# Performance work log

Measured on AMD Instinct MI355X. Metric: run time of the kernel, lower is better.

Reference implementation:

```python
import jax, jax.numpy as jnp
import numpy as np

N, DIM, HEADS, DHEAD = 4096, 1024, 16, 64
INNER = HEADS * DHEAD


def setup_inputs() -> dict:
    key = jax.random.key(0)
    ks = jax.random.split(key, 6)
    s_in = 1.0 / np.sqrt(DIM)
    s_inner = 1.0 / np.sqrt(INNER)
    return {
        "x": jax.random.normal(ks[0], (N, DIM), dtype=jnp.float32),
        # weights stored as (in, out) so y = x @ W
        "Wq": jax.random.uniform(ks[1], (DIM, INNER), jnp.float32, -s_in, s_in),
        "Wk": jax.random.uniform(ks[2], (DIM, INNER), jnp.float32, -s_in, s_in),
        "Wv": jax.random.uniform(ks[3], (DIM, INNER), jnp.float32, -s_in, s_in),
        "Wo": jax.random.uniform(ks[4], (INNER, DIM), jnp.float32, -s_inner, s_inner),
        "bo": jax.random.uniform(ks[5], (DIM,), jnp.float32, -s_inner, s_inner),
    }


def reference(x, Wq, Wk, Wv, Wo, bo):
    scale = DHEAD ** -0.5
    # [n, h, d] -> [h, n, d]
    q = (x @ Wq).reshape(N, HEADS, DHEAD).transpose(1, 0, 2)
    k = (x @ Wk).reshape(N, HEADS, DHEAD).transpose(1, 0, 2)
    v = (x @ Wv).reshape(N, HEADS, DHEAD).transpose(1, 0, 2)
    dots = jnp.einsum("hnd,hmd->hnm", q, k) * scale  # [h, n, n]
    attn = jax.nn.softmax(dots, axis=-1)
    out = jnp.einsum("hnm,hmd->hnd", attn, v)  # [h, n, d]
    out = out.transpose(1, 0, 2).reshape(N, INNER)
    return out @ Wo + bo
```

## Files before the change

### kernel.cpp

```cpp
#include <hip/hip_runtime.h>
#include <cstdint>
#include <cstddef>

typedef _Float16 f16;
typedef _Float16 f16x8 __attribute__((ext_vector_type(8)));
typedef _Float16 f16x4 __attribute__((ext_vector_type(4)));
typedef __fp16 fp16x2 __attribute__((ext_vector_type(2)));
typedef float floatx4 __attribute__((ext_vector_type(4)));
typedef float floatx16 __attribute__((ext_vector_type(16)));

constexpr int SEQ = 4096;
constexpr int DIM = 1024;
constexpr int NHEAD = 16;
constexpr int DH = 64;

#define QSCALE 0.18033688011112042f

__device__ __forceinline__ void async16(void* lds, const void* g) {
  __builtin_amdgcn_global_load_lds(
      (__attribute__((address_space(1))) void*)g,
      (__attribute__((address_space(3))) void*)lds, 16, 0, 0);
}

__device__ __forceinline__ uint32_t pk2(float a, float b) {
  union { fp16x2 h; uint32_t u; } c;
  c.h = __builtin_amdgcn_cvt_pkrtz(a, b);
  return c.u;
}

__device__ __forceinline__ float dot2acc(uint32_t packed, float acc) {
#if __has_builtin(__builtin_amdgcn_fdot2)
  union { uint32_t u; fp16x2 h; } c; c.u = packed;
  fp16x2 one2; one2.x = (__fp16)1.0f; one2.y = (__fp16)1.0f;
  return __builtin_amdgcn_fdot2(c.h, one2, acc, false);
#else
  union { uint32_t u; fp16x2 h; } c; c.u = packed;
  return acc + (float)c.h.x + (float)c.h.y;
#endif
}


__global__ void cvt_x(const float* __restrict__ x, f16* __restrict__ xh) {
  int i = (blockIdx.x * 256 + threadIdx.x) * 4;
  float4 v = *(const float4*)(x + i);
  f16x4 o;
  o.x = (f16)v.x; o.y = (f16)v.y; o.z = (f16)v.z; o.w = (f16)v.w;
  *(f16x4*)(xh + i) = o;
}

__global__ void transpose_cvt(const float* __restrict__ w0, const float* __restrict__ w1,
                              const float* __restrict__ w2, const float* __restrict__ w3,
                              f16* __restrict__ o0, f16* __restrict__ o1,
                              f16* __restrict__ o2, f16* __restrict__ o3) {
  __shared__ float tile[32][33];
  int z = blockIdx.z;
  const float* W = (z == 0) ? w0 : (z == 1) ? w1 : (z == 2) ? w2 : w3;
  f16* O = (z == 0) ? o0 : (z == 1) ? o1 : (z == 2) ? o2 : o3;
  int tx = threadIdx.x, ty = threadIdx.y;
  int xc = blockIdx.x * 32 + tx;
  for (int i = ty; i < 32; i += 8)
    tile[i][tx] = W[(size_t)(blockIdx.y * 32 + i) * DIM + xc];
  __syncthreads();
  int xo = blockIdx.y * 32 + tx;
  for (int i = ty; i < 32; i += 8)
    O[(size_t)(blockIdx.x * 32 + i) * DIM + xo] = (f16)tile[tx][i];
}

__global__ __launch_bounds__(256, 3) void gemm_qkv(
    const f16* __restrict__ xh, const f16* __restrict__ wqt,
    const f16* __restrict__ wkt, const f16* __restrict__ wvt,
    f16* __restrict__ q_ws, f16* __restrict__ k_ws, f16* __restrict__ vt_ws) {
  __shared__ f16 smem[16896];
  f16* a_lds = smem;
  f16* b_lds = smem + 4096;
  const int tid = threadIdx.x;
  const int lane = tid & 63, l16 = lane & 15, quad = lane >> 4;
  const int w = tid >> 6, wr = w >> 1, wc = w & 1;
  const int m0 = blockIdx.x * 128, n0 = blockIdx.y * 128;
  const int z = blockIdx.z;
  const f16* Bt = (z == 0) ? wqt : (z == 1) ? wkt : wvt;

  floatx4 acc[4][4];
#pragma unroll
  for (int mt = 0; mt < 4; ++mt)
#pragma unroll
    for (int nt = 0; nt < 4; ++nt) acc[mt][nt] = (floatx4){0.f, 0.f, 0.f, 0.f};

  for (int k0 = 0; k0 < DIM; k0 += 32) {
#pragma unroll
    for (int rnd = 0; rnd < 2; ++rnd) {
      int e = (rnd * 256 + tid) * 8;
      int cb = e >> 10, r = (e >> 3) & 127;
      async16(a_lds + e, xh + (size_t)(m0 + r) * DIM + k0 + cb * 8);
      async16(b_lds + e, Bt + (size_t)(n0 + r) * DIM + k0 + cb * 8);
    }
    __syncthreads();
    f16x8 af[4], bq[4];
#pragma unroll
    for (int mt = 0; mt < 4; ++mt)
      af[mt] = *(const f16x8*)(a_lds + quad * 1024 + (wr * 64 + mt * 16 + l16) * 8);
#pragma unroll
    for (int nt = 0; nt < 4; ++nt)
      bq[nt] = *(const f16x8*)(b_lds + quad * 1024 + (wc * 64 + nt * 16 + l16) * 8);
#pragma unroll
    for (int mt = 0; mt < 4; ++mt)
#pragma unroll
      for (int nt = 0; nt < 4; ++nt)
        acc[mt][nt] = __builtin_amdgcn_mfma_f32_16x16x32_f16(af[mt], bq[nt], acc[mt][nt], 0, 0, 0);
    __syncthreads();
  }

  if (z < 2) {
#pragma unroll
    for (int mt = 0; mt < 4; ++mt)
#pragma unroll
      for (int nt = 0; nt < 4; ++nt)
#pragma unroll
        for (int r = 0; r < 4; ++r) {
          int m = m0 + wr * 64 + mt * 16 + quad * 4 + r;
          int c = n0 + wc * 64 + nt * 16 + l16;
          float v = acc[mt][nt][r];
          if (z == 0)
            q_ws[(size_t)((c >> 6) * SEQ + m) * DH + (c & 63)] = (f16)(v * QSCALE);
          else
            k_ws[(size_t)((c >> 6) * SEQ + m) * DH + (c & 63)] = (f16)v;
        }
  } else {
#pragma unroll
    for (int mt = 0; mt < 4; ++mt)
#pragma unroll
      for (int nt = 0; nt < 4; ++nt)
#pragma unroll
        for (int r = 0; r < 4; ++r) {
          int cl = wc * 64 + nt * 16 + l16;
          int ml = wr * 64 + mt * 16 + quad * 4 + r;
          smem[cl * 132 + ml] = (f16)acc[mt][nt][r];
        }
    __syncthreads();
#pragma unroll
    for (int it = 0; it < 8; ++it) {
      int idx = it * 256 + tid;
      int cl = idx >> 4, mp = (idx & 15) * 8;
      f16x4 lo = *(const f16x4*)(smem + cl * 132 + mp);
      f16x4 hi4 = *(const f16x4*)(smem + cl * 132 + mp + 4);
      f16x8 v8;
#pragma unroll
      for (int j = 0; j < 4; ++j) { v8[j] = lo[j]; v8[4 + j] = hi4[j]; }
      *(f16x8*)(vt_ws + (size_t)(n0 + cl) * SEQ + m0 + mp) = v8;
    }
  }
}

__global__ __launch_bounds__(256, 4) void attn_kernel(
    const f16* __restrict__ qg, const f16* __restrict__ kg,
    const f16* __restrict__ vtg, f16* __restrict__ po, float* __restrict__ ps) {
  __shared__ f16 smem[16384];
  f16* k_lds = smem;
  f16* v_lds = smem + 8192;

  const int tid = threadIdx.x;
  const int w = tid >> 6, lane = tid & 63, l32 = lane & 31;
  const int hi = lane >> 5;
  const int h = blockIdx.y, qt = blockIdx.x, half = blockIdx.z;
  const int q0 = qt * 128 + w * 32;

  f16x8 qf[4];
#pragma unroll
  for (int kf = 0; kf < 4; ++kf)
    qf[kf] = *(const f16x8*)(qg + (size_t)(h * SEQ + q0 + l32) * DH + kf * 16 + hi * 8);

  floatx16 oacc[2];
  oacc[0] = (floatx16)0.f; oacc[1] = (floatx16)0.f;
  float ssum = 0.f;

  const int kt0 = half * (SEQ / 256), kt1 = kt0 + (SEQ / 256);
  for (int kt = kt0; kt < kt1; ++kt) {
#pragma unroll
    for (int rnd = 0; rnd < 4; ++rnd) {
      int e = (rnd * 256 + tid) * 8;
      {
        int cb = e >> 10, r = (e >> 3) & 127;
        async16(k_lds + e, kg + (size_t)(h * SEQ + kt * 128 + r) * DH + cb * 8);
      }
      {
        int cb = e >> 9, r = (e >> 3) & 63;
        async16(v_lds + e, vtg + (size_t)(h * DH + r) * SEQ + kt * 128 + cb * 8);
      }
    }
    __syncthreads();

#pragma unroll
    for (int kb = 0; kb < 4; ++kb) {
      floatx16 sacc = (floatx16)0.f;
#pragma unroll
      for (int kf = 0; kf < 4; ++kf) {
        f16x8 kfrag = *(const f16x8*)(k_lds + (kf * 2 + hi) * 1024 + (kb * 32 + l32) * 8);
        sacc = __builtin_amdgcn_mfma_f32_32x32x16_f16(kfrag, qf[kf], sacc, 0, 0, 0);
      }
      float p[16];
#pragma unroll
      for (int r = 0; r < 16; ++r) p[r] = exp2f(sacc[r]);
#pragma unroll
      for (int kh = 0; kh < 2; ++kh) {
        uint32_t d0a = pk2(p[8 * kh + 0], p[8 * kh + 1]);
        uint32_t d0b = pk2(p[8 * kh + 2], p[8 * kh + 3]);
        uint32_t d1a = pk2(p[8 * kh + 4], p[8 * kh + 5]);
        uint32_t d1b = pk2(p[8 * kh + 6], p[8 * kh + 7]);
        ssum = dot2acc(d0a, ssum);
        ssum = dot2acc(d0b, ssum);
        ssum = dot2acc(d1a, ssum);
        ssum = dot2acc(d1b, ssum);
        uint32_t ra = (uint32_t)__shfl_xor((int)(hi ? d0a : d1a), 32);
        uint32_t rb = (uint32_t)__shfl_xor((int)(hi ? d0b : d1b), 32);
        union { uint32_t u[4]; f16x8 v; } bu;
        bu.u[0] = hi ? ra : d0a;
        bu.u[1] = hi ? rb : d0b;
        bu.u[2] = hi ? d1a : ra;
        bu.u[3] = hi ? d1b : rb;
        f16x8 bfrag = bu.v;
        int cb = kb * 4 + kh * 2 + hi;
#pragma unroll
        for (int dt = 0; dt < 2; ++dt) {
          f16x8 vfrag = *(const f16x8*)(v_lds + cb * 512 + (dt * 32 + l32) * 8);
          oacc[dt] = __builtin_amdgcn_mfma_f32_32x32x16_f16(vfrag, bfrag, oacc[dt], 0, 0, 0);
        }
      }
    }
    __syncthreads();
  }

  ssum += __shfl_xor(ssum, 32);
  const int tileid = (half * NHEAD + h) * 32 + qt;
  if (hi == 0) ps[(size_t)tileid * 128 + w * 32 + l32] = ssum;

  f16* pob = po + (size_t)tileid * 8192;
#pragma unroll
  for (int dt = 0; dt < 2; ++dt)
#pragma unroll
    for (int r = 0; r < 16; ++r) {
      int d = dt * 32 + (r & 3) + 8 * (r >> 2) + 4 * hi;
      pob[d * 128 + w * 32 + l32] = (f16)oacc[dt][r];
    }
}

__global__ __launch_bounds__(256, 4) void combine(
    const f16* __restrict__ po, const float* __restrict__ ps, f16* __restrict__ og) {
  __shared__ float inv_s[128];
  __shared__ f16 t[128 * 68];
  const int tid = threadIdx.x;
  const int h = blockIdx.y, qt = blockIdx.x;
  const int t0 = h * 32 + qt, t1 = (NHEAD + h) * 32 + qt;
  if (tid < 128) inv_s[tid] = 1.f / (ps[(size_t)t0 * 128 + tid] + ps[(size_t)t1 * 128 + tid]);
  __syncthreads();
  const f16* b0 = po + (size_t)t0 * 8192;
  const f16* b1 = po + (size_t)t1 * 8192;
#pragma unroll
  for (int it = 0; it < 4; ++it) {
    int e = (it * 256 + tid) * 8;
    int d = e >> 7, q = e & 127;
    f16x8 a = *(const f16x8*)(b0 + e);
    f16x8 b = *(const f16x8*)(b1 + e);
#pragma unroll
    for (int j = 0; j < 8; ++j)
      t[(q + j) * 68 + d] = (f16)(((float)a[j] + (float)b[j]) * inv_s[q + j]);
  }
  __syncthreads();
#pragma unroll
  for (int it = 0; it < 4; ++it) {
    int idx = it * 256 + tid;
    int q = idx >> 3, dcol = (idx & 7) * 8;
    f16x4 lo = *(const f16x4*)(t + q * 68 + dcol);
    f16x4 hi4 = *(const f16x4*)(t + q * 68 + dcol + 4);
    f16x8 v8;
#pragma unroll
    for (int j = 0; j < 4; ++j) { v8[j] = lo[j]; v8[4 + j] = hi4[j]; }
    *(f16x8*)(og + (size_t)(qt * 128 + q) * DIM + h * DH + dcol) = v8;
  }
}

__global__ __launch_bounds__(256, 2) void gemm_o(
    const f16* __restrict__ ab, const f16* __restrict__ wot,
    const float* __restrict__ bo, float* __restrict__ out) {
  __shared__ f16 a_lds[4096];
  __shared__ f16 b_lds[2048];
  const int tid = threadIdx.x;
  const int lane = tid & 63, l16 = lane & 15, quad = lane >> 4;
  const int w = tid >> 6, wr = w >> 1, wc = w & 1;
  const int m0 = blockIdx.x * 128, n0 = blockIdx.y * 64;

  floatx4 acc[4][2];
#pragma unroll
  for (int mt = 0; mt < 4; ++mt)
#pragma unroll
    for (int nt = 0; nt < 2; ++nt) acc[mt][nt] = (floatx4){0.f, 0.f, 0.f, 0.f};

  for (int k0 = 0; k0 < DIM; k0 += 32) {
#pragma unroll
    for (int rnd = 0; rnd < 2; ++rnd) {
      int e = (rnd * 256 + tid) * 8;
      int cb = e >> 10, r = (e >> 3) & 127;
      async16(a_lds + e, ab + (size_t)(m0 + r) * DIM + k0 + cb * 8);
    }
    {
      int e = tid * 8;
      int cb = e >> 9, r = (e >> 3) & 63;
      async16(b_lds + e, wot + (size_t)(n0 + r) * DIM + k0 + cb * 8);
    }
    __syncthreads();
    f16x8 af[4], bq[2];
#pragma unroll
    for (int mt = 0; mt < 4; ++mt)
      af[mt] = *(const f16x8*)(a_lds + quad * 1024 + (wr * 64 + mt * 16 + l16) * 8);
#pragma unroll
    for (int nt = 0; nt < 2; ++nt)
      bq[nt] = *(const f16x8*)(b_lds + quad * 512 + (wc * 32 + nt * 16 + l16) * 8);
#pragma unroll
    for (int mt = 0; mt < 4; ++mt)
#pragma unroll
      for (int nt = 0; nt < 2; ++nt)
        acc[mt][nt] = __builtin_amdgcn_mfma_f32_16x16x32_f16(af[mt], bq[nt], acc[mt][nt], 0, 0, 0);
    __syncthreads();
  }

#pragma unroll
  for (int mt = 0; mt < 4; ++mt)
#pragma unroll
    for (int nt = 0; nt < 2; ++nt)
#pragma unroll
      for (int r = 0; r < 4; ++r) {
        int m = m0 + wr * 64 + mt * 16 + quad * 4 + r;
        int c = n0 + wc * 32 + nt * 16 + l16;
        out[(size_t)m * DIM + c] = acc[mt][nt][r] + bo[c];
      }
}


extern "C" void kernel_launch(void* const* d_in, const int* in_sizes, int n_in,
                              void* d_out, int out_size, void* d_ws, size_t ws_size,
                              hipStream_t stream) {
  (void)in_sizes; (void)n_in; (void)out_size; (void)ws_size;
  const float* x  = (const float*)d_in[0];
  const float* Wq = (const float*)d_in[1];
  const float* Wk = (const float*)d_in[2];
  const float* Wv = (const float*)d_in[3];
  const float* Wo = (const float*)d_in[4];
  const float* bo = (const float*)d_in[5];
  float* out = (float*)d_out;
  char* ws = (char*)d_ws;

  f16* xh    = (f16*)(ws);
  f16* wqt   = (f16*)(ws + (8u  << 20));
  f16* wkt   = (f16*)(ws + (10u << 20));
  f16* wvt   = (f16*)(ws + (12u << 20));
  f16* wot   = (f16*)(ws + (14u << 20));
  f16* q_ws  = (f16*)(ws + (16u << 20));
  f16* k_ws  = (f16*)(ws + (24u << 20));
  f16* vt_ws = (f16*)(ws + (32u << 20));
  f16* po    = (f16*)(ws + (40u << 20));
  float* ps  = (float*)(ws + (57u << 20));
  f16* aout  = xh;

  cvt_x<<<dim3(SEQ * DIM / 1024), dim3(256), 0, stream>>>(x, xh);
  transpose_cvt<<<dim3(32, 32, 4), dim3(32, 8), 0, stream>>>(Wq, Wk, Wv, Wo, wqt, wkt, wvt, wot);
  gemm_qkv<<<dim3(32, 8, 3), dim3(256), 0, stream>>>(xh, wqt, wkt, wvt, q_ws, k_ws, vt_ws);
  attn_kernel<<<dim3(SEQ / 128, NHEAD, 2), dim3(256), 0, stream>>>(q_ws, k_ws, vt_ws, po, ps);
  combine<<<dim3(SEQ / 128, NHEAD), dim3(256), 0, stream>>>(po, ps, aout);
  gemm_o<<<dim3(32, 16), dim3(256), 0, stream>>>(aout, wot, bo, out);
}
```

Baseline: 288.7 us.

## Shrink attention query tile to 64 and split key blocks across warps

The attention kernel now processes 64 queries per block instead of 128. Its four warps form a 2x2 grid over queries and keys, and each iteration streams a 64-key chunk. Partial outputs and softmax sums from the two key-split warps are reduced through shared memory before writing. The combine kernel is resized to match. This doubles the grid, halves LDS per block and raises occupancy. The cost is more K/V reloads per query, since each K/V tile is now shared by only 64 queries, plus an extra LDS reduction and sync at the end.

New measurement: 532.3 us. 1.84x slower.

```diff
diff --git a/kernel.cpp b/kernel.cpp
--- a/kernel.cpp
+++ b/kernel.cpp
@@ -151,113 +151,123 @@
   }
 }
 
-__global__ __launch_bounds__(256, 4) void attn_kernel(
+__global__ __launch_bounds__(256, 8) void attn_kernel(
     const f16* __restrict__ qg, const f16* __restrict__ kg,
     const f16* __restrict__ vtg, f16* __restrict__ po, float* __restrict__ ps) {
-  __shared__ f16 smem[16384];
+  __shared__ f16 smem[8448];
   f16* k_lds = smem;
-  f16* v_lds = smem + 8192;
+  f16* v_lds = smem + 4096;
 
   const int tid = threadIdx.x;
   const int w = tid >> 6, lane = tid & 63, l32 = lane & 31;
   const int hi = lane >> 5;
+  const int wq = w & 1, wk = w >> 1;
   const int h = blockIdx.y, qt = blockIdx.x, half = blockIdx.z;
-  const int q0 = qt * 128 + w * 32;
 
   f16x8 qf[4];
 #pragma unroll
   for (int kf = 0; kf < 4; ++kf)
-    qf[kf] = *(const f16x8*)(qg + (size_t)(h * SEQ + q0 + l32) * DH + kf * 16 + hi * 8);
+    qf[kf] = *(const f16x8*)(qg + (size_t)(h * SEQ + qt * 64 + wq * 32 + l32) * DH +
+                             kf * 16 + hi * 8);
 
   floatx16 oacc[2];
   oacc[0] = (floatx16)0.f; oacc[1] = (floatx16)0.f;
   float ssum = 0.f;
 
-  const int kt0 = half * (SEQ / 256), kt1 = kt0 + (SEQ / 256);
-  for (int kt = kt0; kt < kt1; ++kt) {
-#pragma unroll
-    for (int rnd = 0; rnd < 4; ++rnd) {
+  const int kk0 = half * (SEQ / 2);
+  for (int kt = 0; kt < 32; ++kt) {
+    const int kk = kk0 + kt * 64;
+#pragma unroll
+    for (int rnd = 0; rnd < 2; ++rnd) {
       int e = (rnd * 256 + tid) * 8;
-      {
-        int cb = e >> 10, r = (e >> 3) & 127;
-        async16(k_lds + e, kg + (size_t)(h * SEQ + kt * 128 + r) * DH + cb * 8);
+      int cb = e >> 9, r = (e >> 3) & 63;
+      async16(k_lds + e, kg + (size_t)(h * SEQ + kk + r) * DH + cb * 8);
+      async16(v_lds + e, vtg + (size_t)(h * DH + r) * SEQ + kk + cb * 8);
+    }
+    __syncthreads();
+
+    floatx16 sacc = (floatx16)0.f;
+#pragma unroll
+    for (int kf = 0; kf < 4; ++kf) {
+      f16x8 kfrag = *(const f16x8*)(k_lds + (kf * 2 + hi) * 512 + (wk * 32 + l32) * 8);
+      sacc = __builtin_amdgcn_mfma_f32_32x32x16_f16(kfrag, qf[kf], sacc, 0, 0, 0);
+    }
+    float p[16];
+#pragma unroll
+    for (int r = 0; r < 16; ++r) p[r] = exp2f(sacc[r]);
+#pragma unroll
+    for (int kh = 0; kh < 2; ++kh) {
+      uint32_t d0a = pk2(p[8 * kh + 0], p[8 * kh + 1]);
+      uint32_t d0b = pk2(p[8 * kh + 2], p[8 * kh + 3]);
+      uint32_t d1a = pk2(p[8 * kh + 4], p[8 * kh + 5]);
+      uint32_t d1b = pk2(p[8 * kh + 6], p[8 * kh + 7]);
+      ssum = dot2acc(d0a, ssum);
+      ssum = dot2acc(d0b, ssum);
+      ssum = dot2acc(d1a, ssum);
+      ssum = dot2acc(d1b, ssum);
+      uint32_t ra = (uint32_t)__shfl_xor((int)(hi ? d0a : d1a), 32);
+      uint32_t rb = (uint32_t)__shfl_xor((int)(hi ? d0b : d1b), 32);
+      union { uint32_t u[4]; f16x8 v; } bu;
+      bu.u[0] = hi ? ra : d0a;
+      bu.u[1] = hi ? rb : d0b;
+      bu.u[2] = hi ? d1a : ra;
+      bu.u[3] = hi ? d1b : rb;
+      f16x8 bfrag = bu.v;
+      int cb = wk * 4 + kh * 2 + hi;
+#pragma unroll
+      for (int dt = 0; dt < 2; ++dt) {
+        f16x8 vfrag = *(const f16x8*)(v_lds + cb * 512 + (dt * 32 + l32) * 8);
+        oacc[dt] = __builtin_amdgcn_mfma_f32_32x32x16_f16(vfrag, bfrag, oacc[dt], 0, 0, 0);
       }
-      {
-        int cb = e >> 9, r = (e >> 3) & 63;
-        async16(v_lds + e, vtg + (size_t)(h * DH + r) * SEQ + kt * 128 + cb * 8);
+    }
+    __syncthreads();
+  }
+
+  ssum += __shfl_xor(ssum, 32);
+
+  float* oF = (float*)smem;
+  float* ssums = oF + 4160;
+  if (wk == 1) {
+#pragma unroll
+    for (int dt = 0; dt < 2; ++dt)
+#pragma unroll
+      for (int r = 0; r < 16; ++r) {
+        int d = dt * 32 + (r & 3) + 8 * (r >> 2) + 4 * hi;
+        oF[(wq * 32 + l32) * 65 + d] = oacc[dt][r];
       }
-    }
-    __syncthreads();
-
-#pragma unroll
-    for (int kb = 0; kb < 4; ++kb) {
-      floatx16 sacc = (floatx16)0.f;
-#pragma unroll
-      for (int kf = 0; kf < 4; ++kf) {
-        f16x8 kfrag = *(const f16x8*)(k_lds + (kf * 2 + hi) * 1024 + (kb * 32 + l32) * 8);
-        sacc = __builtin_amdgcn_mfma_f32_32x32x16_f16(kfrag, qf[kf], sacc, 0, 0, 0);
+    if (hi == 0) ssums[wq * 32 + l32] = ssum;
+  }
+  __syncthreads();
+  if (wk == 0) {
+    const int tileid = (half * NHEAD + h) * 64 + qt;
+    f16* pob = po + (size_t)tileid * 4096;
+    int q = wq * 32 + l32;
+#pragma unroll
+    for (int dt = 0; dt < 2; ++dt)
+#pragma unroll
+      for (int r = 0; r < 16; ++r) {
+        int d = dt * 32 + (r & 3) + 8 * (r >> 2) + 4 * hi;
+        pob[d * 64 + q] = (f16)(oacc[dt][r] + oF[q * 65 + d]);
       }
-      float p[16];
-#pragma unroll
-      for (int r = 0; r < 16; ++r) p[r] = exp2f(sacc[r]);
-#pragma unroll
-      for (int kh = 0; kh < 2; ++kh) {
-        uint32_t d0a = pk2(p[8 * kh + 0], p[8 * kh + 1]);
-        uint32_t d0b = pk2(p[8 * kh + 2], p[8 * kh + 3]);
-        uint32_t d1a = pk2(p[8 * kh + 4], p[8 * kh + 5]);
-        uint32_t d1b = pk2(p[8 * kh + 6], p[8 * kh + 7]);
-        ssum = dot2acc(d0a, ssum);
-        ssum = dot2acc(d0b, ssum);
-        ssum = dot2acc(d1a, ssum);
-        ssum = dot2acc(d1b, ssum);
-        uint32_t ra = (uint32_t)__shfl_xor((int)(hi ? d0a : d1a), 32);
-        uint32_t rb = (uint32_t)__shfl_xor((int)(hi ? d0b : d1b), 32);
-        union { uint32_t u[4]; f16x8 v; } bu;
-        bu.u[0] = hi ? ra : d0a;
-        bu.u[1] = hi ? rb : d0b;
-        bu.u[2] = hi ? d1a : ra;
-        bu.u[3] = hi ? d1b : rb;
-        f16x8 bfrag = bu.v;
-        int cb = kb * 4 + kh * 2 + hi;
-#pragma unroll
-        for (int dt = 0; dt < 2; ++dt) {
-          f16x8 vfrag = *(const f16x8*)(v_lds + cb * 512 + (dt * 32 + l32) * 8);
-          oacc[dt] = __builtin_amdgcn_mfma_f32_32x32x16_f16(vfrag, bfrag, oacc[dt], 0, 0, 0);
-        }
-      }
-    }
-    __syncthreads();
-  }
-
-  ssum += __shfl_xor(ssum, 32);
-  const int tileid = (half * NHEAD + h) * 32 + qt;
-  if (hi == 0) ps[(size_t)tileid * 128 + w * 32 + l32] = ssum;
-
-  f16* pob = po + (size_t)tileid * 8192;
-#pragma unroll
-  for (int dt = 0; dt < 2; ++dt)
-#pragma unroll
-    for (int r = 0; r < 16; ++r) {
-      int d = dt * 32 + (r & 3) + 8 * (r >> 2) + 4 * hi;
-      pob[d * 128 + w * 32 + l32] = (f16)oacc[dt][r];
-    }
-}
-
-__global__ __launch_bounds__(256, 4) void combine(
+    if (hi == 0) ps[(size_t)tileid * 64 + q] = ssum + ssums[q];
+  }
+}
+
+__global__ __launch_bounds__(256, 8) void combine(
     const f16* __restrict__ po, const float* __restrict__ ps, f16* __restrict__ og) {
-  __shared__ float inv_s[128];
-  __shared__ f16 t[128 * 68];
+  __shared__ float inv_s[64];
+  __shared__ f16 t[64 * 68];
   const int tid = threadIdx.x;
   const int h = blockIdx.y, qt = blockIdx.x;
-  const int t0 = h * 32 + qt, t1 = (NHEAD + h) * 32 + qt;
-  if (tid < 128) inv_s[tid] = 1.f / (ps[(size_t)t0 * 128 + tid] + ps[(size_t)t1 * 128 + tid]);
+  const int t0 = h * 64 + qt, t1 = (NHEAD + h) * 64 + qt;
+  if (tid < 64) inv_s[tid] = 1.f / (ps[(size_t)t0 * 64 + tid] + ps[(size_t)t1 * 64 + tid]);
   __syncthreads();
-  const f16* b0 = po + (size_t)t0 * 8192;
-  const f16* b1 = po + (size_t)t1 * 8192;
-#pragma unroll
-  for (int it = 0; it < 4; ++it) {
+  const f16* b0 = po + (size_t)t0 * 4096;
+  const f16* b1 = po + (size_t)t1 * 4096;
+#pragma unroll
+  for (int it = 0; it < 2; ++it) {
     int e = (it * 256 + tid) * 8;
-    int d = e >> 7, q = e & 127;
+    int d = e >> 6, q = e & 63;
     f16x8 a = *(const f16x8*)(b0 + e);
     f16x8 b = *(const f16x8*)(b1 + e);
 #pragma unroll
@@ -266,7 +276,7 @@
   }
   __syncthreads();
 #pragma unroll
-  for (int it = 0; it < 4; ++it) {
+  for (int it = 0; it < 2; ++it) {
     int idx = it * 256 + tid;
     int q = idx >> 3, dcol = (idx & 7) * 8;
     f16x4 lo = *(const f16x4*)(t + q * 68 + dcol);
@@ -274,7 +284,7 @@
     f16x8 v8;
 #pragma unroll
     for (int j = 0; j < 4; ++j) { v8[j] = lo[j]; v8[4 + j] = hi4[j]; }
-    *(f16x8*)(og + (size_t)(qt * 128 + q) * DIM + h * DH + dcol) = v8;
+    *(f16x8*)(og + (size_t)(qt * 64 + q) * DIM + h * DH + dcol) = v8;
   }
 }
 
@@ -363,7 +373,7 @@
   cvt_x<<<dim3(SEQ * DIM / 1024), dim3(256), 0, stream>>>(x, xh);
   transpose_cvt<<<dim3(32, 32, 4), dim3(32, 8), 0, stream>>>(Wq, Wk, Wv, Wo, wqt, wkt, wvt, wot);
   gemm_qkv<<<dim3(32, 8, 3), dim3(256), 0, stream>>>(xh, wqt, wkt, wvt, q_ws, k_ws, vt_ws);
-  attn_kernel<<<dim3(SEQ / 128, NHEAD, 2), dim3(256), 0, stream>>>(q_ws, k_ws, vt_ws, po, ps);
-  combine<<<dim3(SEQ / 128, NHEAD), dim3(256), 0, stream>>>(po, ps, aout);
+  attn_kernel<<<dim3(SEQ / 64, NHEAD, 2), dim3(256), 0, stream>>>(q_ws, k_ws, vt_ws, po, ps);
+  combine<<<dim3(SEQ / 64, NHEAD), dim3(256), 0, stream>>>(po, ps, aout);
   gemm_o<<<dim3(32, 16), dim3(256), 0, stream>>>(aout, wot, bo, out);
 }
```

## Split attention key tile across two wave groups with 512-thread blocks

Applied to the files above, without the earlier changes.

The attention kernel now runs 512 threads per block. Two groups of four waves each take half of every 128-key tile, which halves the serial per-wave work along the key dimension and raises waves per CU. The partial outputs and row sums of the two groups are reduced through LDS before the single global write. In exchange, each block now does an extra LDS reduction and barrier at the end, and the launch bounds change, which tightens the register budget per thread.

Result: slower. 549.2 us (+90.3%).

```diff
diff --git a/kernel.cpp b/kernel.cpp
--- a/kernel.cpp
+++ b/kernel.cpp
@@ -151,7 +151,7 @@
   }
 }
 
-__global__ __launch_bounds__(256, 4) void attn_kernel(
+__global__ __launch_bounds__(512, 8) void attn_kernel(
     const f16* __restrict__ qg, const f16* __restrict__ kg,
     const f16* __restrict__ vtg, f16* __restrict__ po, float* __restrict__ ps) {
   __shared__ f16 smem[16384];
@@ -161,40 +161,44 @@
   const int tid = threadIdx.x;
   const int w = tid >> 6, lane = tid & 63, l32 = lane & 31;
   const int hi = lane >> 5;
+  const int wq = w & 3, wk = w >> 2;
   const int h = blockIdx.y, qt = blockIdx.x, half = blockIdx.z;
-  const int q0 = qt * 128 + w * 32;
+  const int q = wq * 32 + l32;
 
   f16x8 qf[4];
 #pragma unroll
   for (int kf = 0; kf < 4; ++kf)
-    qf[kf] = *(const f16x8*)(qg + (size_t)(h * SEQ + q0 + l32) * DH + kf * 16 + hi * 8);
+    qf[kf] = *(const f16x8*)(qg + (size_t)(h * SEQ + qt * 128 + q) * DH +
+                             kf * 16 + hi * 8);
 
   floatx16 oacc[2];
   oacc[0] = (floatx16)0.f; oacc[1] = (floatx16)0.f;
   float ssum = 0.f;
 
-  const int kt0 = half * (SEQ / 256), kt1 = kt0 + (SEQ / 256);
-  for (int kt = kt0; kt < kt1; ++kt) {
-#pragma unroll
-    for (int rnd = 0; rnd < 4; ++rnd) {
-      int e = (rnd * 256 + tid) * 8;
+  const int kk0 = half * (SEQ / 2);
+  for (int kt = 0; kt < 16; ++kt) {
+    const int kk = kk0 + kt * 128;
+#pragma unroll
+    for (int rnd = 0; rnd < 2; ++rnd) {
+      int e = (rnd * 512 + tid) * 8;
       {
         int cb = e >> 10, r = (e >> 3) & 127;
-        async16(k_lds + e, kg + (size_t)(h * SEQ + kt * 128 + r) * DH + cb * 8);
+        async16(k_lds + e, kg + (size_t)(h * SEQ + kk + r) * DH + cb * 8);
       }
       {
         int cb = e >> 9, r = (e >> 3) & 63;
-        async16(v_lds + e, vtg + (size_t)(h * DH + r) * SEQ + kt * 128 + cb * 8);
-      }
-    }
-    __syncthreads();
-
-#pragma unroll
-    for (int kb = 0; kb < 4; ++kb) {
+        async16(v_lds + e, vtg + (size_t)(h * DH + r) * SEQ + kk + cb * 8);
+      }
+    }
+    __syncthreads();
+
+#pragma unroll
+    for (int kb = 0; kb < 2; ++kb) {
       floatx16 sacc = (floatx16)0.f;
 #pragma unroll
       for (int kf = 0; kf < 4; ++kf) {
-        f16x8 kfrag = *(const f16x8*)(k_lds + (kf * 2 + hi) * 1024 + (kb * 32 + l32) * 8);
+        f16x8 kfrag = *(const f16x8*)(k_lds + (kf * 2 + hi) * 1024 +
+                                      (wk * 64 + kb * 32 + l32) * 8);
         sacc = __builtin_amdgcn_mfma_f32_32x32x16_f16(kfrag, qf[kf], sacc, 0, 0, 0);
       }
       float p[16];
@@ -218,7 +222,7 @@
         bu.u[2] = hi ? d1a : ra;
         bu.u[3] = hi ? d1b : rb;
         f16x8 bfrag = bu.v;
-        int cb = kb * 4 + kh * 2 + hi;
+        int cb = wk * 8 + kb * 4 + kh * 2 + hi;
 #pragma unroll
         for (int dt = 0; dt < 2; ++dt) {
           f16x8 vfrag = *(const f16x8*)(v_lds + cb * 512 + (dt * 32 + l32) * 8);
@@ -230,17 +234,32 @@
   }
 
   ssum += __shfl_xor(ssum, 32);
-  const int tileid = (half * NHEAD + h) * 32 + qt;
-  if (hi == 0) ps[(size_t)tileid * 128 + w * 32 + l32] = ssum;
-
-  f16* pob = po + (size_t)tileid * 8192;
-#pragma unroll
-  for (int dt = 0; dt < 2; ++dt)
-#pragma unroll
-    for (int r = 0; r < 16; ++r) {
-      int d = dt * 32 + (r & 3) + 8 * (r >> 2) + 4 * hi;
-      pob[d * 128 + w * 32 + l32] = (f16)oacc[dt][r];
-    }
+
+  f16* t16 = smem;
+  float* ssums = (float*)(smem + 8704);
+  if (wk == 1) {
+#pragma unroll
+    for (int dt = 0; dt < 2; ++dt)
+#pragma unroll
+      for (int r = 0; r < 16; ++r) {
+        int d = dt * 32 + (r & 3) + 8 * (r >> 2) + 4 * hi;
+        t16[q * 68 + d] = (f16)oacc[dt][r];
+      }
+    if (hi == 0) ssums[q] = ssum;
+  }
+  __syncthreads();
+  if (wk == 0) {
+    const int tileid = (half * NHEAD + h) * 32 + qt;
+    f16* pob = po + (size_t)tileid * 8192;
+#pragma unroll
+    for (int dt = 0; dt < 2; ++dt)
+#pragma unroll
+      for (int r = 0; r < 16; ++r) {
+        int d = dt * 32 + (r & 3) + 8 * (r >> 2) + 4 * hi;
+        pob[d * 128 + q] = (f16)(oacc[dt][r] + (float)t16[q * 68 + d]);
+      }
+    if (hi == 0) ps[(size_t)tileid * 128 + q] = ssum + ssums[q];
+  }
 }
 
 __global__ __launch_bounds__(256, 4) void combine(
@@ -363,7 +382,7 @@
   cvt_x<<<dim3(SEQ * DIM / 1024), dim3(256), 0, stream>>>(x, xh);
   transpose_cvt<<<dim3(32, 32, 4), dim3(32, 8), 0, stream>>>(Wq, Wk, Wv, Wo, wqt, wkt, wvt, wot);
   gemm_qkv<<<dim3(32, 8, 3), dim3(256), 0, stream>>>(xh, wqt, wkt, wvt, q_ws, k_ws, vt_ws);
-  attn_kernel<<<dim3(SEQ / 128, NHEAD, 2), dim3(256), 0, stream>>>(q_ws, k_ws, vt_ws, po, ps);
+  attn_kernel<<<dim3(SEQ / 128, NHEAD, 2), dim3(512), 0, stream>>>(q_ws, k_ws, vt_ws, po, ps);
   combine<<<dim3(SEQ / 128, NHEAD), dim3(256), 0, stream>>>(po, ps, aout);
   gemm_o<<<dim3(32, 16), dim3(256), 0, stream>>>(aout, wot, bo, out);
 }
```
